# Optimization experiments

Hardware: AMD Instinct MI355X
Metric: run time of the kernel (lower is better)

Reference implementation:

```python
import jax, jax.numpy as jnp
import numpy as np

D = 1024
H = 16
HD = D // H
EPS = 1e-5


def layer_norm(x, g, b):
    mu = jnp.mean(x, axis=-1, keepdims=True)
    var = jnp.var(x, axis=-1, keepdims=True)
    return (x - mu) * jax.lax.rsqrt(var + EPS) * g + b


def setup_inputs() -> dict:
    key = jax.random.key(0)
    ks = jax.random.split(key, 16)
    s = 0.02
    return {
        "x": jax.random.normal(ks[0], (2, 2048, D), jnp.float32),
        "ln1_g": jnp.ones((D,), jnp.float32),
        "ln1_b": jnp.zeros((D,), jnp.float32),
        "Wq": jax.random.normal(ks[1], (D, D), jnp.float32) * s,
        "bq": jnp.zeros((D,), jnp.float32),
        "Wk": jax.random.normal(ks[2], (D, D), jnp.float32) * s,
        "bk": jnp.zeros((D,), jnp.float32),
        "Wv": jax.random.normal(ks[3], (D, D), jnp.float32) * s,
        "bv": jnp.zeros((D,), jnp.float32),
        "Wo": jax.random.normal(ks[4], (D, D), jnp.float32) * s,
        "bo": jnp.zeros((D,), jnp.float32),
        "ln2_g": jnp.ones((D,), jnp.float32),
        "ln2_b": jnp.zeros((D,), jnp.float32),
        "W1": jax.random.normal(ks[5], (D, 4 * D), jnp.float32) * s,
        "b1": jnp.zeros((4 * D,), jnp.float32),
        "W2": jax.random.normal(ks[6], (4 * D, D), jnp.float32) * s,
        "b2": jnp.zeros((D,), jnp.float32),
    }


def reference(x, ln1_g, ln1_b, Wq, bq, Wk, bk, Wv, bv, Wo, bo, ln2_g, ln2_b, W1, b1, W2, b2):
    B, T, _ = x.shape
    # --- attention sub-block (pre-LN) ---
    h = layer_norm(x, ln1_g, ln1_b)
    q = (h @ Wq + bq).reshape(B, T, H, HD).transpose(0, 2, 1, 3)  # [B,H,T,hd]
    k = (h @ Wk + bk).reshape(B, T, H, HD).transpose(0, 2, 1, 3)
    v = (h @ Wv + bv).reshape(B, T, H, HD).transpose(0, 2, 1, 3)
    scores = jnp.einsum("bhqd,bhkd->bhqk", q, k)  # full O(T^2) scores as in source
    causal = jnp.tril(jnp.ones((T, T), bool))
    scores = jnp.where(causal, scores, -jnp.inf)
    w = jax.nn.softmax(scores / np.sqrt(HD), axis=-1)
    ctx = jnp.einsum("bhqk,bhkd->bhqd", w, v)
    ctx = ctx.transpose(0, 2, 1, 3).reshape(B, T, D)
    x = x + (ctx @ Wo + bo)
    # --- MLP sub-block (pre-LN) ---
    h = layer_norm(x, ln2_g, ln2_b)
    h = jax.nn.gelu(h @ W1 + b1, approximate=False)
    x = x + (h @ W2 + b2)
    return x
```

## Files before the change

### kernel.cpp

```cpp
#include <hip/hip_runtime.h>
#include <math.h>


typedef _Float16 half8 __attribute__((ext_vector_type(8)));
typedef _Float16 half4v __attribute__((ext_vector_type(4)));
typedef float floatx4 __attribute__((ext_vector_type(4)));

#define DMODEL 1024
#define SEQT   2048
#define NTOK   4096
#define NHEAD  16
#define HDIM   64

__device__ __forceinline__ void llds16(const _Float16* g, _Float16* l) {
  __builtin_amdgcn_global_load_lds(
      (const __attribute__((address_space(1))) void*)g,
      (__attribute__((address_space(3))) void*)l, 16, 0, 0);
}

__global__ __launch_bounds__(256) void wtrans_kernel(
    const float* __restrict__ Wq, const float* __restrict__ Wk,
    const float* __restrict__ Wv, const float* __restrict__ Wo,
    const float* __restrict__ W1, const float* __restrict__ W2,
    _Float16* __restrict__ wt_base) {
  __shared__ float tilebuf[32][33];
  int id = blockIdx.x;
  const float* src; _Float16* dst; int K, N, t;
  if (id < 4096) {
    int s = id >> 10;
    src = (s == 0) ? Wq : (s == 1) ? Wk : (s == 2) ? Wv : Wo;
    dst = wt_base + (size_t)s * (1024 * 1024);
    K = 1024; N = 1024; t = id & 1023;
  } else if (id < 8192) {
    src = W1; dst = wt_base + (size_t)4 * 1024 * 1024; K = 1024; N = 4096; t = id - 4096;
  } else {
    src = W2; dst = wt_base + (size_t)8 * 1024 * 1024; K = 4096; N = 1024; t = id - 8192;
  }
  int tilesN = N >> 5;
  int tk = t / tilesN, tn = t % tilesN;
  int c = threadIdx.x & 31, r0 = threadIdx.x >> 5;
#pragma unroll
  for (int i = 0; i < 4; ++i) {
    int r = r0 + i * 8;
    tilebuf[r][c] = src[(size_t)(tk * 32 + r) * N + tn * 32 + c];
  }
  __syncthreads();
#pragma unroll
  for (int i = 0; i < 4; ++i) {
    int r = r0 + i * 8;
    dst[(size_t)(tn * 32 + r) * K + tk * 32 + c] = (_Float16)tilebuf[c][r];
  }
}

__global__ __launch_bounds__(256) void ln_kernel(
    const float* __restrict__ x, const float* __restrict__ g,
    const float* __restrict__ b, _Float16* __restrict__ out) {
  int row = blockIdx.x;
  int t = threadIdx.x;
  const float4 xv = ((const float4*)(x + (size_t)row * DMODEL))[t];
  float s = xv.x + xv.y + xv.z + xv.w;
  float s2 = xv.x * xv.x + xv.y * xv.y + xv.z * xv.z + xv.w * xv.w;
#pragma unroll
  for (int off = 32; off; off >>= 1) {
    s += __shfl_down(s, off);
    s2 += __shfl_down(s2, off);
  }
  __shared__ float red[8];
  int wid = t >> 6;
  if ((t & 63) == 0) { red[wid] = s; red[wid + 4] = s2; }
  __syncthreads();
  s = red[0] + red[1] + red[2] + red[3];
  s2 = red[4] + red[5] + red[6] + red[7];
  float mu = s * (1.0f / DMODEL);
  float var = s2 * (1.0f / DMODEL) - mu * mu;
  float rstd = rsqrtf(var + 1e-5f);
  const float4 gv = ((const float4*)g)[t];
  const float4 bv = ((const float4*)b)[t];
  half4v o;
  o[0] = (_Float16)((xv.x - mu) * rstd * gv.x + bv.x);
  o[1] = (_Float16)((xv.y - mu) * rstd * gv.y + bv.y);
  o[2] = (_Float16)((xv.z - mu) * rstd * gv.z + bv.z);
  o[3] = (_Float16)((xv.w - mu) * rstd * gv.w + bv.w);
  *(half4v*)(out + (size_t)row * DMODEL + t * 4) = o;
}

template <int MODE>
__global__ __launch_bounds__(256) void gemm_kernel(
    const _Float16* __restrict__ A, const _Float16* __restrict__ Bt0, int K,
    const float* __restrict__ bias0, const float* __restrict__ bias1,
    const float* __restrict__ bias2, const float* __restrict__ res,
    float* __restrict__ outf, _Float16* __restrict__ outh) {
  __shared__ __align__(16) _Float16 As[2][128 * 32];
  __shared__ __align__(16) _Float16 Bs[2][128 * 32];
  const int tid = threadIdx.x;
  const int m0 = blockIdx.x * 128;
  const _Float16* Bt;
  const float* bias;
  _Float16* outh_sel = outh;
  int n0, sel = 0;
  if (MODE == 0) {
    sel = blockIdx.y >> 3;
    n0 = (blockIdx.y & 7) * 128;
    Bt = Bt0 + (size_t)sel * (1024 * 1024);
    bias = (sel == 0) ? bias0 : (sel == 1) ? bias1 : bias2;
    outh_sel = outh + (size_t)sel * ((size_t)NTOK * DMODEL);
  } else {
    n0 = blockIdx.y * 128;
    Bt = Bt0;
    bias = bias0;
  }
  int Keff = K, koff = 0;
  if (MODE == 3) { Keff = K >> 1; koff = blockIdx.z * Keff; }
  const int w = tid >> 6, lane = tid & 63;
  const int l15 = lane & 15, q8 = lane >> 4;
  const int wrow = (w >> 1) * 64;
  const int wcol = (w & 1) * 64;
  const int csw = (q8 ^ ((l15 >> 1) & 3)) * 8;

  const _Float16* gA[2]; const _Float16* gB[2]; int ldsc[2];
#pragma unroll
  for (int i = 0; i < 2; ++i) {
    int idx = i * 256 + w * 64 + lane;
    int m = idx >> 2;
    int kq = ((idx & 3) ^ ((m >> 1) & 3)) * 8;
    gA[i] = A + (size_t)(m0 + m) * K + koff + kq;
    gB[i] = Bt + (size_t)(n0 + m) * K + koff + kq;
    ldsc[i] = idx * 8;
  }

  auto stage = [&](int buf) {
#pragma unroll
    for (int i = 0; i < 2; ++i) {
      llds16(gA[i], &As[buf][ldsc[i]]);
      gA[i] += 32;
    }
#pragma unroll
    for (int i = 0; i < 2; ++i) {
      llds16(gB[i], &Bs[buf][ldsc[i]]);
      gB[i] += 32;
    }
  };

  floatx4 acc[4][4];
#pragma unroll
  for (int i = 0; i < 4; ++i)
#pragma unroll
    for (int j = 0; j < 4; ++j) acc[i][j] = (floatx4){0.f, 0.f, 0.f, 0.f};

  const int nk = Keff >> 5;
  stage(0);
  __syncthreads();
  for (int t = 0; t < nk; ++t) {
    const int buf = t & 1;
    if (t + 1 < nk) stage(buf ^ 1);
    half8 af[4], bf[4];
#pragma unroll
    for (int i = 0; i < 4; ++i)
      af[i] = *(const half8*)&As[buf][(wrow + i * 16 + l15) * 32 + csw];
#pragma unroll
    for (int j = 0; j < 4; ++j)
      bf[j] = *(const half8*)&Bs[buf][(wcol + j * 16 + l15) * 32 + csw];
#pragma unroll
    for (int i = 0; i < 4; ++i)
#pragma unroll
      for (int j = 0; j < 4; ++j)
        acc[i][j] = __builtin_amdgcn_mfma_f32_16x16x32_f16(af[i], bf[j], acc[i][j], 0, 0, 0);
    __syncthreads();
  }

#pragma unroll
  for (int i = 0; i < 4; ++i) {
    int rowb = m0 + wrow + i * 16 + q8 * 4;
#pragma unroll
    for (int j = 0; j < 4; ++j) {
      int col = n0 + wcol + j * 16 + l15;
      float bval = bias[col];
#pragma unroll
      for (int r = 0; r < 4; ++r) {
        int row = rowb + r;
        float v = acc[i][j][r];
        if (MODE == 0) {
          v += bval;
          int bb = row >> 11, tt = row & 2047;
          int hh = col >> 6, hd = col & 63;
          if (sel == 2)
            outh_sel[((size_t)(bb * NHEAD + hh) * HDIM + hd) * SEQT + tt] = (_Float16)v;
          else
            outh_sel[((size_t)(bb * NHEAD + hh) * SEQT + tt) * HDIM + hd] = (_Float16)v;
        } else if (MODE == 1) {
          v += bval + res[(size_t)row * 1024 + col];
          outf[(size_t)row * 1024 + col] = v;
        } else if (MODE == 2) {
          v += bval;
          float z = 1.5957691216f * v * (1.0f + 0.044715f * v * v);
          float gl = v / (1.0f + __expf(-z));
          outh[(size_t)row * 4096 + col] = (_Float16)gl;
        } else {
          if (blockIdx.z == 0) v += bval + res[(size_t)row * 1024 + col];
          unsafeAtomicAdd(outf + (size_t)row * 1024 + col, v);
        }
      }
    }
  }
}

__global__ __launch_bounds__(256) void attn_kernel(
    const _Float16* __restrict__ q, const _Float16* __restrict__ k,
    const _Float16* __restrict__ vt, _Float16* __restrict__ ctx) {
  __shared__ __align__(16) _Float16 Ks[2][64 * 64];
  __shared__ __align__(16) _Float16 Vs[2][64 * 64];
  __shared__ __align__(16) _Float16 Ps[64 * 72];
  __shared__ float Lpart[4][64];
  const int tid = threadIdx.x;
  const int w = tid >> 6, lane = tid & 63;
  const int l15 = lane & 15, q8 = lane >> 4;
  const int bh = blockIdx.y;
  const int pr = blockIdx.x;
  const size_t base = (size_t)bh * SEQT * HDIM;

  const _Float16* gk0[2]; const _Float16* gv0[2]; int ldsc[2];
#pragma unroll
  for (int i = 0; i < 2; ++i) {
    int c = i * 256 + w * 64 + lane;
    int r = c >> 3, gc = ((c & 7) ^ (r & 7)) * 8;
    gk0[i] = k + base + (size_t)r * HDIM + gc;
    gv0[i] = vt + base + (size_t)r * SEQT + gc;
    ldsc[i] = c * 8;
  }
  auto stage = [&](int kt, int buf) {
#pragma unroll
    for (int i = 0; i < 2; ++i) {
      llds16(gk0[i] + (size_t)kt * (64 * HDIM), &Ks[buf][ldsc[i]]);
      llds16(gv0[i] + kt * 64, &Vs[buf][ldsc[i]]);
    }
  };

  const int rswA = (l15 & 7);
  const int cs0 = (q8 ^ rswA) * 8;
  const int cs1 = ((4 + q8) ^ rswA) * 8;

  int s = 0;
  stage(0, 0);
  __syncthreads();
  for (int ph = 0; ph < 2; ++ph) {
    const int qtile = ph ? 31 - pr : pr;
    const int ntile = qtile + 1;
    half8 bq[4][2];
#pragma unroll
    for (int nt = 0; nt < 4; ++nt) {
      const half8* qp = (const half8*)(q + base + (size_t)(qtile * 64 + nt * 16 + l15) * HDIM);
      bq[nt][0] = qp[q8];
      bq[nt][1] = qp[4 + q8];
    }
    floatx4 acc[4];
#pragma unroll
    for (int j = 0; j < 4; ++j) acc[j] = (floatx4){0.f, 0.f, 0.f, 0.f};
    float lsum[4] = {0.f, 0.f, 0.f, 0.f};

    for (int jt = 0; jt < ntile; ++jt, ++s) {
      const int buf = s & 1;
      if (s + 1 < 33) {
        int sn = s + 1;
        int nkt = (sn <= pr) ? sn : sn - (pr + 1);
        stage(nkt, buf ^ 1);
      }
      half8 ak0 = *(const half8*)&Ks[buf][(w * 16 + l15) * 64 + cs0];
      half8 ak1 = *(const half8*)&Ks[buf][(w * 16 + l15) * 64 + cs1];
      floatx4 sv[4];
#pragma unroll
      for (int nt = 0; nt < 4; ++nt) {
        sv[nt] = __builtin_amdgcn_mfma_f32_16x16x32_f16(ak0, bq[nt][0],
                                                        (floatx4){0.f, 0.f, 0.f, 0.f}, 0, 0, 0);
        sv[nt] = __builtin_amdgcn_mfma_f32_16x16x32_f16(ak1, bq[nt][1], sv[nt], 0, 0, 0);
      }
      const bool diag = (jt == ntile - 1);
#pragma unroll
      for (int nt = 0; nt < 4; ++nt) {
        half4v phv;
#pragma unroll
        for (int r = 0; r < 4; ++r) {
          float p = __expf(sv[nt][r] * 0.125f);
          if (diag) {
            p = (w * 16 + q8 * 4 + r <= nt * 16 + l15) ? p : 0.f;
          }
          lsum[nt] += p;
          phv[r] = (_Float16)p;
        }
        *(half4v*)&Ps[(nt * 16 + l15) * 72 + w * 16 + q8 * 4] = phv;
      }
      __syncthreads();
      half8 ap0 = *(const half8*)&Ps[(w * 16 + l15) * 72 + q8 * 8];
      half8 ap1 = *(const half8*)&Ps[(w * 16 + l15) * 72 + 32 + q8 * 8];
#pragma unroll
      for (int ntd = 0; ntd < 4; ++ntd) {
        half8 bv0 = *(const half8*)&Vs[buf][(ntd * 16 + l15) * 64 + cs0];
        half8 bv1 = *(const half8*)&Vs[buf][(ntd * 16 + l15) * 64 + cs1];
        acc[ntd] = __builtin_amdgcn_mfma_f32_16x16x32_f16(ap0, bv0, acc[ntd], 0, 0, 0);
        acc[ntd] = __builtin_amdgcn_mfma_f32_16x16x32_f16(ap1, bv1, acc[ntd], 0, 0, 0);
      }
      __syncthreads();
    }

#pragma unroll
    for (int nt = 0; nt < 4; ++nt) {
      lsum[nt] += __shfl_xor(lsum[nt], 16);
      lsum[nt] += __shfl_xor(lsum[nt], 32);
      if (q8 == 0) Lpart[w][nt * 16 + l15] = lsum[nt];
    }
    __syncthreads();
    const int b = bh >> 4, h = bh & 15;
#pragma unroll
    for (int r = 0; r < 4; ++r) {
      int qr = w * 16 + q8 * 4 + r;
      float inv = 1.0f / (Lpart[0][qr] + Lpart[1][qr] + Lpart[2][qr] + Lpart[3][qr]);
      int tg = qtile * 64 + qr;
      _Float16* op = ctx + ((size_t)(b * SEQT + tg)) * DMODEL + h * HDIM;
#pragma unroll
      for (int ntd = 0; ntd < 4; ++ntd)
        op[ntd * 16 + l15] = (_Float16)(acc[ntd][r] * inv);
    }
  }
}

extern "C" void kernel_launch(void* const* d_in, const int* in_sizes, int n_in,
                              void* d_out, int out_size, void* d_ws, size_t ws_size,
                              hipStream_t stream) {
  (void)in_sizes; (void)n_in; (void)out_size; (void)ws_size;
  const float* x    = (const float*)d_in[0];
  const float* ln1g = (const float*)d_in[1];
  const float* ln1b = (const float*)d_in[2];
  const float* Wq   = (const float*)d_in[3];
  const float* bq   = (const float*)d_in[4];
  const float* Wk   = (const float*)d_in[5];
  const float* bk   = (const float*)d_in[6];
  const float* Wv   = (const float*)d_in[7];
  const float* bv   = (const float*)d_in[8];
  const float* Wo   = (const float*)d_in[9];
  const float* bo   = (const float*)d_in[10];
  const float* ln2g = (const float*)d_in[11];
  const float* ln2b = (const float*)d_in[12];
  const float* W1   = (const float*)d_in[13];
  const float* b1   = (const float*)d_in[14];
  const float* W2   = (const float*)d_in[15];
  const float* b2   = (const float*)d_in[16];
  float* out = (float*)d_out;

  char* ws = (char*)d_ws;
  _Float16* wt    = (_Float16*)(ws);
  _Float16* h16   = (_Float16*)(ws + ((size_t)24 << 20));
  _Float16* qkv   = (_Float16*)(ws + ((size_t)32 << 20));
  _Float16* ctx16 = (_Float16*)(ws + ((size_t)24 << 20));
  float*    x1    = (float*)   (ws + ((size_t)32 << 20));
  _Float16* h2    = (_Float16*)(ws + ((size_t)48 << 20));
  _Float16* mid   = (_Float16*)(ws + ((size_t)56 << 20));

  const size_t QKV1 = (size_t)NTOK * DMODEL;

  wtrans_kernel<<<12288, 256, 0, stream>>>(Wq, Wk, Wv, Wo, W1, W2, wt);
  ln_kernel<<<NTOK, 256, 0, stream>>>(x, ln1g, ln1b, h16);
  gemm_kernel<0><<<dim3(32, 24), 256, 0, stream>>>(
      h16, wt, 1024, bq, bk, bv, nullptr, nullptr, qkv);
  attn_kernel<<<dim3(16, 32), 256, 0, stream>>>(
      qkv, qkv + QKV1, qkv + 2 * QKV1, ctx16);
  gemm_kernel<1><<<dim3(32, 8), 256, 0, stream>>>(
      ctx16, wt + (size_t)3 * 1024 * 1024, 1024, bo, nullptr, nullptr, x, x1, nullptr);
  ln_kernel<<<NTOK, 256, 0, stream>>>(x1, ln2g, ln2b, h2);
  gemm_kernel<2><<<dim3(32, 32), 256, 0, stream>>>(
      h2, wt + (size_t)4 * 1024 * 1024, 1024, b1, nullptr, nullptr, nullptr, nullptr, mid);
  hipMemsetAsync(out, 0, (size_t)NTOK * DMODEL * sizeof(float), stream);
  gemm_kernel<3><<<dim3(32, 8, 2), 256, 0, stream>>>(
      mid, wt + (size_t)8 * 1024 * 1024, 4096, b2, nullptr, nullptr, x1, out, nullptr);
}
```

Baseline: 382.0 us.

## Triple-buffer GEMM LDS pipeline and drop split-K atomics for final projection

```diff
diff --git a/kernel.cpp b/kernel.cpp
--- a/kernel.cpp
+++ b/kernel.cpp
@@ -11,6 +11,13 @@
 #define NTOK   4096
 #define NHEAD  16
 #define HDIM   64
+
+#define FULL_BARRIER()                      \
+  do {                                      \
+    asm volatile("" ::: "memory");          \
+    __builtin_amdgcn_s_barrier();           \
+    asm volatile("" ::: "memory");          \
+  } while (0)
 
 __device__ __forceinline__ void llds16(const _Float16* g, _Float16* l) {
   __builtin_amdgcn_global_load_lds(
@@ -90,8 +97,8 @@
     const float* __restrict__ bias0, const float* __restrict__ bias1,
     const float* __restrict__ bias2, const float* __restrict__ res,
     float* __restrict__ outf, _Float16* __restrict__ outh) {
-  __shared__ __align__(16) _Float16 As[2][128 * 32];
-  __shared__ __align__(16) _Float16 Bs[2][128 * 32];
+  __shared__ __align__(16) _Float16 As[3][128 * 32];
+  __shared__ __align__(16) _Float16 Bs[3][128 * 32];
   const int tid = threadIdx.x;
   const int m0 = blockIdx.x * 128;
   const _Float16* Bt;
@@ -109,8 +116,6 @@
     Bt = Bt0;
     bias = bias0;
   }
-  int Keff = K, koff = 0;
-  if (MODE == 3) { Keff = K >> 1; koff = blockIdx.z * Keff; }
   const int w = tid >> 6, lane = tid & 63;
   const int l15 = lane & 15, q8 = lane >> 4;
   const int wrow = (w >> 1) * 64;
@@ -123,8 +128,8 @@
     int idx = i * 256 + w * 64 + lane;
     int m = idx >> 2;
     int kq = ((idx & 3) ^ ((m >> 1) & 3)) * 8;
-    gA[i] = A + (size_t)(m0 + m) * K + koff + kq;
-    gB[i] = Bt + (size_t)(n0 + m) * K + koff + kq;
+    gA[i] = A + (size_t)(m0 + m) * K + kq;
+    gB[i] = Bt + (size_t)(n0 + m) * K + kq;
     ldsc[i] = idx * 8;
   }
 
@@ -147,25 +152,35 @@
 #pragma unroll
     for (int j = 0; j < 4; ++j) acc[i][j] = (floatx4){0.f, 0.f, 0.f, 0.f};
 
-  const int nk = Keff >> 5;
+  const int nk = K >> 5;
   stage(0);
-  __syncthreads();
+  stage(1);
+  int rb = 0;
   for (int t = 0; t < nk; ++t) {
-    const int buf = t & 1;
-    if (t + 1 < nk) stage(buf ^ 1);
+    if (t + 2 < nk) {
+      int wb = rb - 1; if (wb < 0) wb += 3;
+      stage(wb);
+      asm volatile("s_waitcnt vmcnt(8)" ::: "memory");
+    } else if (t + 1 < nk) {
+      asm volatile("s_waitcnt vmcnt(4)" ::: "memory");
+    } else {
+      asm volatile("s_waitcnt vmcnt(0)" ::: "memory");
+    }
+    FULL_BARRIER();
     half8 af[4], bf[4];
 #pragma unroll
     for (int i = 0; i < 4; ++i)
-      af[i] = *(const half8*)&As[buf][(wrow + i * 16 + l15) * 32 + csw];
+      af[i] = *(const half8*)&As[rb][(wrow + i * 16 + l15) * 32 + csw];
 #pragma unroll
     for (int j = 0; j < 4; ++j)
-      bf[j] = *(const half8*)&Bs[buf][(wcol + j * 16 + l15) * 32 + csw];
+      bf[j] = *(const half8*)&Bs[rb][(wcol + j * 16 + l15) * 32 + csw];
 #pragma unroll
     for (int i = 0; i < 4; ++i)
 #pragma unroll
       for (int j = 0; j < 4; ++j)
         acc[i][j] = __builtin_amdgcn_mfma_f32_16x16x32_f16(af[i], bf[j], acc[i][j], 0, 0, 0);
-    __syncthreads();
+    FULL_BARRIER();
+    if (++rb == 3) rb = 0;
   }
 
 #pragma unroll
@@ -178,9 +193,8 @@
 #pragma unroll
       for (int r = 0; r < 4; ++r) {
         int row = rowb + r;
-        float v = acc[i][j][r];
+        float v = acc[i][j][r] + bval;
         if (MODE == 0) {
-          v += bval;
           int bb = row >> 11, tt = row & 2047;
           int hh = col >> 6, hd = col & 63;
           if (sel == 2)
@@ -188,16 +202,12 @@
           else
             outh_sel[((size_t)(bb * NHEAD + hh) * SEQT + tt) * HDIM + hd] = (_Float16)v;
         } else if (MODE == 1) {
-          v += bval + res[(size_t)row * 1024 + col];
+          v += res[(size_t)row * 1024 + col];
           outf[(size_t)row * 1024 + col] = v;
-        } else if (MODE == 2) {
-          v += bval;
+        } else {
           float z = 1.5957691216f * v * (1.0f + 0.044715f * v * v);
           float gl = v / (1.0f + __expf(-z));
           outh[(size_t)row * 4096 + col] = (_Float16)gl;
-        } else {
-          if (blockIdx.z == 0) v += bval + res[(size_t)row * 1024 + col];
-          unsafeAtomicAdd(outf + (size_t)row * 1024 + col, v);
         }
       }
     }
@@ -367,7 +377,6 @@
   ln_kernel<<<NTOK, 256, 0, stream>>>(x1, ln2g, ln2b, h2);
   gemm_kernel<2><<<dim3(32, 32), 256, 0, stream>>>(
       h2, wt + (size_t)4 * 1024 * 1024, 1024, b1, nullptr, nullptr, nullptr, nullptr, mid);
-  hipMemsetAsync(out, 0, (size_t)NTOK * DMODEL * sizeof(float), stream);
-  gemm_kernel<3><<<dim3(32, 8, 2), 256, 0, stream>>>(
+  gemm_kernel<1><<<dim3(32, 8), 256, 0, stream>>>(
       mid, wt + (size_t)8 * 1024 * 1024, 4096, b2, nullptr, nullptr, x1, out, nullptr);
 }
```

New measurement: 380.4 us. About the same (-0.4%).
